# Performance work log

Hardware: AMD Instinct MI355X
Metric: run time of the kernel (lower is better)

The kernel has to match this reference:

```python
import jax, jax.numpy as jnp
import numpy as np


def setup_inputs() -> dict:
    key = jax.random.key(0)
    k1, k2, k3 = jax.random.split(key, 3)
    B, C, H, W = 512, 4, 125, 125
    img = jax.random.normal(k1, (B, C, H, W), dtype=jnp.float32)
    # fc: Linear(62500 -> 20), Tanh, Dropout(eval=identity), Linear(20 -> 1), Sigmoid
    W1 = jax.random.normal(k2, (C * H * W, 20), dtype=jnp.float32) * 0.004  # ~1/sqrt(62500)
    b1 = jnp.zeros((20,), dtype=jnp.float32)
    W2 = jax.random.normal(k3, (20, 1), dtype=jnp.float32) * 0.2
    b2 = jnpp = jnp.zeros((1,), dtype=jnp.float32)
    return {"img": img, "W1": W1, "b1": b1, "W2": W2, "b2": b2}


def reference(img, W1, b1, W2, b2):
    B, C, H, W = img.shape
    # small MLP -> rotation angle theta in [0, 2*pi)
    h = jnp.tanh(img.reshape(B, -1) @ W1 + b1)          # (B, 20)
    theta = jax.nn.sigmoid(h @ W2 + b2)[:, 0] * (2.0 * np.pi)  # (B,)
    c, s = jnp.cos(theta), jnp.sin(theta)
    z = jnp.zeros_like(c)
    # (B, 2, 3) affine matrix: pure rotation, zero translation
    Mat = jnp.stack([jnp.stack([c, -s, z], axis=-1),
                     jnp.stack([s,  c, z], axis=-1)], axis=-2)

    # affine_grid, align_corners=True: normalized coords span [-1, 1] at pixel centers
    ys = jnp.linspace(-1.0, 1.0, H, dtype=img.dtype)
    xs = jnp.linspace(-1.0, 1.0, W, dtype=img.dtype)
    gy, gx = jnp.meshgrid(ys, xs, indexing="ij")        # (H, W)
    base = jnp.stack([gx, gy, jnp.ones_like(gx)], axis=-1)  # (H, W, 3) homogeneous (x, y, 1)
    grid = jnp.einsum("bij,hwj->bhwi", Mat, base)       # (B, H, W, 2) -> (x, y)

    # grid_sample: bilinear, padding_mode='zeros', align_corners=True
    ix = (grid[..., 0] + 1.0) * 0.5 * (W - 1)
    iy = (grid[..., 1] + 1.0) * 0.5 * (H - 1)
    ix0 = jnp.floor(ix); iy0 = jnp.floor(iy)
    ix1 = ix0 + 1.0;     iy1 = iy0 + 1.0
    wx1 = ix - ix0; wx0 = 1.0 - wx1
    wy1 = iy - iy0; wy0 = 1.0 - wy1

    def gather(ixi, iyi):
        valid = (ixi >= 0) & (ixi <= W - 1) & (iyi >= 0) & (iyi <= H - 1)
        xc = jnp.clip(ixi, 0, W - 1).astype(jnp.int32)
        yc = jnp.clip(iyi, 0, H - 1).astype(jnp.int32)
        vals = jax.vmap(lambda im, yy, xx: im[:, yy, xx])(img, yc, xc)  # (B, C, H, W)
        return vals * valid[:, None, :, :].astype(img.dtype)

    out = (gather(ix0, iy0) * (wx0 * wy0)[:, None]
         + gather(ix1, iy0) * (wx1 * wy0)[:, None]
         + gather(ix0, iy1) * (wx0 * wy1)[:, None]
         + gather(ix1, iy1) * (wx1 * wy1)[:, None])
    return out, Mat
```

## Files before the change

kernel.cpp:

```cpp
#include <hip/hip_runtime.h>
#include <hip/hip_bf16.h>
#include <math.h>

#define K_TOT 62500
#define KQ_TOT 15625
#define NJ    20
#define NB    512
#define HW_   15625
#define WW_   125
#define NKSPL 128
#define LDSTR 68
#define SWSTR 124

#define HP_OFF   0
#define HRED_OFF (NKSPL * NJ * NB)
#define W1T_OFF  2000000
#define MAT_OFF  32000000

__global__ __launch_bounds__(256) void k0_transpose(const float* __restrict__ W1,
                                                    float* __restrict__ W1T) {
    const int k = blockIdx.x * 256 + threadIdx.x;
    if (k >= K_TOT) return;
    const float* src = W1 + (size_t)k * NJ;
#pragma unroll
    for (int j = 0; j < NJ; ++j)
        W1T[(size_t)j * K_TOT + k] = src[j];
}

__global__ __launch_bounds__(256, 2) void k1_partial(const float* __restrict__ img,
                                                     const float* __restrict__ W1T,
                                                     float* __restrict__ hpart) {
    __shared__ float  simg[2][64 * LDSTR];
    __shared__ float4 sw[NJ * SWSTR];
    const int tid  = threadIdx.x;
    const int bx   = blockIdx.x;
    const int b0   = blockIdx.y << 6;
    const int lane = tid & 63;
    const int j0   = __builtin_amdgcn_readfirstlane((tid >> 6) * 5);
    const int srow = tid >> 4;
    const int squad = tid & 15;

    const int q0  = (bx * KQ_TOT) >> 7;
    const int q1  = ((bx + 1) * KQ_TOT) >> 7;
    const int nqb = q1 - q0;
    const int nsteps = (nqb + 15) >> 4;

    const float4* img4 = reinterpret_cast<const float4*>(img);
    const float4* W1T4 = reinterpret_cast<const float4*>(W1T);

    for (int i = tid; i < NJ * 128; i += 256) {
        const int j  = i >> 7;
        const int qq = i & 127;
        if (qq < nqb)
            sw[j * SWSTR + qq] = W1T4[(size_t)j * KQ_TOT + q0 + qq];
    }

    float acc0 = 0.f, acc1 = 0.f, acc2 = 0.f, acc3 = 0.f, acc4 = 0.f;

    {
        const int cq = (nqb < 16) ? nqb : 16;
        if (squad < cq) {
            const int qg = q0 + squad;
#pragma unroll
            for (int rr = 0; rr < 4; ++rr) {
                const int row = srow + (rr << 4);
                *reinterpret_cast<float4*>(&simg[0][row * LDSTR + (squad << 2)]) =
                    img4[(size_t)(b0 + row) * KQ_TOT + qg];
            }
        }
    }
    __syncthreads();

    int cur = 0;
    for (int s = 0; s < nsteps; ++s) {
        float4 r0, r1, r2, r3;
        bool dl = false;
        if (s + 1 < nsteps) {
            const int rem = nqb - (s + 1) * 16;
            const int cq  = (rem < 16) ? rem : 16;
            if (squad < cq) {
                dl = true;
                const size_t qg = (size_t)q0 + (s + 1) * 16 + squad;
                r0 = img4[(size_t)(b0 + srow +  0) * KQ_TOT + qg];
                r1 = img4[(size_t)(b0 + srow + 16) * KQ_TOT + qg];
                r2 = img4[(size_t)(b0 + srow + 32) * KQ_TOT + qg];
                r3 = img4[(size_t)(b0 + srow + 48) * KQ_TOT + qg];
            }
        }

        {
            const int rem = nqb - s * 16;
            const int cq  = (rem < 16) ? rem : 16;
            const float* simgl = &simg[cur][lane * LDSTR];
            const int qbase = s * 16;
#pragma unroll 4
            for (int q = 0; q < cq; ++q) {
                const float4 iv = *reinterpret_cast<const float4*>(&simgl[q << 2]);
                const int qi = qbase + q;
                const float4 w0 = sw[(j0 + 0) * SWSTR + qi];
                const float4 w1 = sw[(j0 + 1) * SWSTR + qi];
                const float4 w2 = sw[(j0 + 2) * SWSTR + qi];
                const float4 w3 = sw[(j0 + 3) * SWSTR + qi];
                const float4 w4 = sw[(j0 + 4) * SWSTR + qi];
                acc0 += iv.x * w0.x + iv.y * w0.y + iv.z * w0.z + iv.w * w0.w;
                acc1 += iv.x * w1.x + iv.y * w1.y + iv.z * w1.z + iv.w * w1.w;
                acc2 += iv.x * w2.x + iv.y * w2.y + iv.z * w2.z + iv.w * w2.w;
                acc3 += iv.x * w3.x + iv.y * w3.y + iv.z * w3.z + iv.w * w3.w;
                acc4 += iv.x * w4.x + iv.y * w4.y + iv.z * w4.z + iv.w * w4.w;
            }
        }

        if (dl) {
            float* d = &simg[cur ^ 1][srow * LDSTR + (squad << 2)];
            *reinterpret_cast<float4*>(&d[ 0 * LDSTR]) = r0;
            *reinterpret_cast<float4*>(&d[16 * LDSTR]) = r1;
            *reinterpret_cast<float4*>(&d[32 * LDSTR]) = r2;
            *reinterpret_cast<float4*>(&d[48 * LDSTR]) = r3;
        }
        __syncthreads();
        cur ^= 1;
    }

    const int b = b0 + lane;
    float* dst = &hpart[(size_t)(bx * NJ + j0) * NB + b];
    dst[0 * NB] = acc0;
    dst[1 * NB] = acc1;
    dst[2 * NB] = acc2;
    dst[3 * NB] = acc3;
    dst[4 * NB] = acc4;
}

__global__ __launch_bounds__(256) void k2_reduce(const float* __restrict__ hpart,
                                                 float* __restrict__ hred) {
    const int b = blockIdx.x * 256 + threadIdx.x;
    const int j = blockIdx.y;
    float a = 0.f;
#pragma unroll 8
    for (int c = 0; c < NKSPL; ++c)
        a += hpart[(size_t)(c * NJ + j) * NB + b];
    hred[j * NB + b] = a;
}

__global__ __launch_bounds__(256) void k2_head(const float* __restrict__ hred,
                                               const float* __restrict__ b1,
                                               const float* __restrict__ W2,
                                               const float* __restrict__ b2,
                                               float* __restrict__ mat) {
    const int b = blockIdx.x * 256 + threadIdx.x;
    float z = b2[0];
#pragma unroll
    for (int j = 0; j < NJ; ++j) {
        const float h = tanhf(hred[j * NB + b] + b1[j]);
        z += h * W2[j];
    }
    const float sg = 1.0f / (1.0f + expf(-z));
    const float theta = sg * 6.28318530717958647692f;
    float sn, cn;
    sincosf(theta, &sn, &cn);
    float* m = mat + (size_t)b * 6;
    m[0] = cn; m[1] = -sn; m[2] = 0.f;
    m[3] = sn; m[4] = cn;  m[5] = 0.f;
}

__device__ __forceinline__ unsigned int pack2bf(float a, float b) {
    __hip_bfloat16 ha = __float2bfloat16(a);
    __hip_bfloat16 hb = __float2bfloat16(b);
    const unsigned int ua = (unsigned int)__builtin_bit_cast(unsigned short, ha);
    const unsigned int ub = (unsigned int)__builtin_bit_cast(unsigned short, hb);
    return ua | (ub << 16);
}
#define BF_LO(u) __uint_as_float((u) << 16)
#define BF_HI(u) __uint_as_float((u) & 0xffff0000u)

__global__ __launch_bounds__(1024) void k3_sample(const float* __restrict__ img,
                                                  const float* __restrict__ mat,
                                                  float* __restrict__ out) {
    __shared__ unsigned int sch[HW_];
    const int b   = blockIdx.x;
    const int tid = threadIdx.x;

    const float cb = mat[(size_t)b * 6 + 4];
    const float sb = mat[(size_t)b * 6 + 3];
    const size_t ib = (size_t)b * 4 * HW_;

#pragma unroll
    for (int pair = 0; pair < 2; ++pair) {
        const float* pa = img + ib + (size_t)(2 * pair) * HW_;
        const float* pb = pa + HW_;
        __syncthreads();
        for (int i = tid; i < HW_; i += 1024)
            sch[i] = pack2bf(pa[i], pb[i]);
        __syncthreads();

        float* oa = out + ib + (size_t)(2 * pair) * HW_;
        for (int p = tid; p < HW_; p += 1024) {
            const int y = p / WW_;
            const int x = p - y * WW_;

            const float gx = (float)x * (1.0f / 62.0f) - 1.0f;
            const float gy = (float)y * (1.0f / 62.0f) - 1.0f;
            const float fx = (cb * gx - sb * gy + 1.0f) * 62.0f;
            const float fy = (sb * gx + cb * gy + 1.0f) * 62.0f;

            const float x0f = floorf(fx), y0f = floorf(fy);
            const int x0 = (int)x0f, y0 = (int)y0f;
            const int x1 = x0 + 1, y1 = y0 + 1;
            const float wx1 = fx - x0f, wx0 = 1.0f - wx1;
            const float wy1 = fy - y0f, wy0 = 1.0f - wy1;

            const bool vx0 = ((unsigned)x0 <= 124u);
            const bool vx1 = ((unsigned)x1 <= 124u);
            const bool vy0 = ((unsigned)y0 <= 124u);
            const bool vy1 = ((unsigned)y1 <= 124u);

            const int cx0 = min(max(x0, 0), 124), cx1 = min(max(x1, 0), 124);
            const int cy0 = min(max(y0, 0), 124), cy1 = min(max(y1, 0), 124);

            const float m00 = (vx0 && vy0) ? wx0 * wy0 : 0.f;
            const float m01 = (vx1 && vy0) ? wx1 * wy0 : 0.f;
            const float m10 = (vx0 && vy1) ? wx0 * wy1 : 0.f;
            const float m11 = (vx1 && vy1) ? wx1 * wy1 : 0.f;

            const unsigned int q00 = sch[cy0 * WW_ + cx0];
            const unsigned int q01 = sch[cy0 * WW_ + cx1];
            const unsigned int q10 = sch[cy1 * WW_ + cx0];
            const unsigned int q11 = sch[cy1 * WW_ + cx1];

            float a0, a1;
            a0  = BF_LO(q00) * m00;  a1  = BF_HI(q00) * m00;
            a0 += BF_LO(q01) * m01;  a1 += BF_HI(q01) * m01;
            a0 += BF_LO(q10) * m10;  a1 += BF_HI(q10) * m10;
            a0 += BF_LO(q11) * m11;  a1 += BF_HI(q11) * m11;

            oa[p]       = a0;
            oa[p + HW_] = a1;
        }
    }
}

extern "C" void kernel_launch(void* const* d_in, const int* in_sizes, int n_in,
                              void* d_out, int out_size, void* d_ws, size_t ws_size,
                              hipStream_t stream) {
    const float* img = (const float*)d_in[0];
    const float* W1  = (const float*)d_in[1];
    const float* b1  = (const float*)d_in[2];
    const float* W2  = (const float*)d_in[3];
    const float* b2  = (const float*)d_in[4];
    float* out = (float*)d_out;

    float* hpart = out + HP_OFF;
    float* hred  = out + HRED_OFF;
    float* W1T   = out + W1T_OFF;
    float* mat   = out + MAT_OFF;

    hipLaunchKernelGGL(k0_transpose, dim3((K_TOT + 255) / 256), dim3(256), 0, stream, W1, W1T);
    hipLaunchKernelGGL(k1_partial, dim3(NKSPL, 8), dim3(256), 0, stream, img, W1T, hpart);
    hipLaunchKernelGGL(k2_reduce, dim3(2, NJ), dim3(256), 0, stream, hpart, hred);
    hipLaunchKernelGGL(k2_head, dim3(2), dim3(256), 0, stream, hred, b1, W2, b2, mat);
    hipLaunchKernelGGL(k3_sample, dim3(NB), dim3(1024), 0, stream, img, mat, out);
}
```

Before: 125.3 us.

## Pack W1 per group, read weights from global, split sampler across channel pairs

The weight transpose becomes a pack into four groups of five outputs each, interleaved per k. The GEMV kernel then reads weights straight from global memory (wave-uniform addresses) instead of staging them in LDS, which frees LDS so occupancy can rise to four blocks. The sampler launches one block per (batch, channel pair) instead of looping over both pairs, doubling the grid and removing a barrier round. The risk is more global/L2 weight traffic per block, and the first-stage load guard was dropped, which assumes each chunk has at least 16 quads.

```diff
diff --git a/kernel.cpp b/kernel.cpp
--- a/kernel.cpp
+++ b/kernel.cpp
@@ -10,63 +10,57 @@
 #define WW_   125
 #define NKSPL 128
 #define LDSTR 68
-#define SWSTR 124
+#define WPG   312500
 
 #define HP_OFF   0
 #define HRED_OFF (NKSPL * NJ * NB)
-#define W1T_OFF  2000000
+#define W1P_OFF  2000000
 #define MAT_OFF  32000000
 
-__global__ __launch_bounds__(256) void k0_transpose(const float* __restrict__ W1,
-                                                    float* __restrict__ W1T) {
+__global__ __launch_bounds__(256) void k0_pack(const float* __restrict__ W1,
+                                               float* __restrict__ W1P) {
     const int k = blockIdx.x * 256 + threadIdx.x;
     if (k >= K_TOT) return;
     const float* src = W1 + (size_t)k * NJ;
 #pragma unroll
-    for (int j = 0; j < NJ; ++j)
-        W1T[(size_t)j * K_TOT + k] = src[j];
-}
-
-__global__ __launch_bounds__(256, 2) void k1_partial(const float* __restrict__ img,
-                                                     const float* __restrict__ W1T,
+    for (int g = 0; g < 4; ++g) {
+        float* d = W1P + (size_t)g * WPG + (size_t)k * 5;
+#pragma unroll
+        for (int r = 0; r < 5; ++r)
+            d[r] = src[5 * g + r];
+    }
+}
+
+__global__ __launch_bounds__(256, 4) void k1_partial(const float* __restrict__ img,
+                                                     const float* __restrict__ W1P,
                                                      float* __restrict__ hpart) {
-    __shared__ float  simg[2][64 * LDSTR];
-    __shared__ float4 sw[NJ * SWSTR];
+    __shared__ float simg[2][64 * LDSTR];
     const int tid  = threadIdx.x;
     const int bx   = blockIdx.x;
     const int b0   = blockIdx.y << 6;
     const int lane = tid & 63;
-    const int j0   = __builtin_amdgcn_readfirstlane((tid >> 6) * 5);
+    const int jg   = __builtin_amdgcn_readfirstlane(tid >> 6);
+    const int j0   = jg * 5;
     const int srow = tid >> 4;
     const int squad = tid & 15;
 
-    const int q0  = (bx * KQ_TOT) >> 7;
-    const int q1  = ((bx + 1) * KQ_TOT) >> 7;
+    const int q0  = (int)(((long long)bx * KQ_TOT) >> 7);
+    const int q1  = (int)(((long long)(bx + 1) * KQ_TOT) >> 7);
     const int nqb = q1 - q0;
     const int nsteps = (nqb + 15) >> 4;
 
     const float4* img4 = reinterpret_cast<const float4*>(img);
-    const float4* W1T4 = reinterpret_cast<const float4*>(W1T);
-
-    for (int i = tid; i < NJ * 128; i += 256) {
-        const int j  = i >> 7;
-        const int qq = i & 127;
-        if (qq < nqb)
-            sw[j * SWSTR + qq] = W1T4[(size_t)j * KQ_TOT + q0 + qq];
-    }
+    const float4* wg4 = reinterpret_cast<const float4*>(W1P + (size_t)jg * WPG);
 
     float acc0 = 0.f, acc1 = 0.f, acc2 = 0.f, acc3 = 0.f, acc4 = 0.f;
 
     {
-        const int cq = (nqb < 16) ? nqb : 16;
-        if (squad < cq) {
-            const int qg = q0 + squad;
-#pragma unroll
-            for (int rr = 0; rr < 4; ++rr) {
-                const int row = srow + (rr << 4);
-                *reinterpret_cast<float4*>(&simg[0][row * LDSTR + (squad << 2)]) =
-                    img4[(size_t)(b0 + row) * KQ_TOT + qg];
-            }
+        const int qg = q0 + squad;
+#pragma unroll
+        for (int rr = 0; rr < 4; ++rr) {
+            const int row = srow + (rr << 4);
+            *reinterpret_cast<float4*>(&simg[0][row * LDSTR + (squad << 2)]) =
+                img4[(size_t)(b0 + row) * KQ_TOT + qg];
         }
     }
     __syncthreads();
@@ -92,21 +86,24 @@
             const int rem = nqb - s * 16;
             const int cq  = (rem < 16) ? rem : 16;
             const float* simgl = &simg[cur][lane * LDSTR];
-            const int qbase = s * 16;
-#pragma unroll 4
+            const int qb = q0 + s * 16;
+#pragma unroll 16
             for (int q = 0; q < cq; ++q) {
                 const float4 iv = *reinterpret_cast<const float4*>(&simgl[q << 2]);
-                const int qi = qbase + q;
-                const float4 w0 = sw[(j0 + 0) * SWSTR + qi];
-                const float4 w1 = sw[(j0 + 1) * SWSTR + qi];
-                const float4 w2 = sw[(j0 + 2) * SWSTR + qi];
-                const float4 w3 = sw[(j0 + 3) * SWSTR + qi];
-                const float4 w4 = sw[(j0 + 4) * SWSTR + qi];
-                acc0 += iv.x * w0.x + iv.y * w0.y + iv.z * w0.z + iv.w * w0.w;
-                acc1 += iv.x * w1.x + iv.y * w1.y + iv.z * w1.z + iv.w * w1.w;
-                acc2 += iv.x * w2.x + iv.y * w2.y + iv.z * w2.z + iv.w * w2.w;
-                acc3 += iv.x * w3.x + iv.y * w3.y + iv.z * w3.z + iv.w * w3.w;
-                acc4 += iv.x * w4.x + iv.y * w4.y + iv.z * w4.z + iv.w * w4.w;
+                const float4* wq = wg4 + (size_t)(qb + q) * 5;
+                const float4 w0 = wq[0];
+                const float4 w1 = wq[1];
+                const float4 w2 = wq[2];
+                const float4 w3 = wq[3];
+                const float4 w4 = wq[4];
+                acc0 += iv.x * w0.x;  acc1 += iv.x * w0.y;  acc2 += iv.x * w0.z;
+                acc3 += iv.x * w0.w;  acc4 += iv.x * w1.x;
+                acc0 += iv.y * w1.y;  acc1 += iv.y * w1.z;  acc2 += iv.y * w1.w;
+                acc3 += iv.y * w2.x;  acc4 += iv.y * w2.y;
+                acc0 += iv.z * w2.z;  acc1 += iv.z * w2.w;  acc2 += iv.z * w3.x;
+                acc3 += iv.z * w3.y;  acc4 += iv.z * w3.z;
+                acc0 += iv.w * w3.w;  acc1 += iv.w * w4.x;  acc2 += iv.w * w4.y;
+                acc3 += iv.w * w4.z;  acc4 += iv.w * w4.w;
             }
         }
 
@@ -176,65 +173,62 @@
                                                   const float* __restrict__ mat,
                                                   float* __restrict__ out) {
     __shared__ unsigned int sch[HW_];
-    const int b   = blockIdx.x;
-    const int tid = threadIdx.x;
+    const int b    = blockIdx.x;
+    const int pair = blockIdx.y;
+    const int tid  = threadIdx.x;
 
     const float cb = mat[(size_t)b * 6 + 4];
     const float sb = mat[(size_t)b * 6 + 3];
     const size_t ib = (size_t)b * 4 * HW_;
-
-#pragma unroll
-    for (int pair = 0; pair < 2; ++pair) {
-        const float* pa = img + ib + (size_t)(2 * pair) * HW_;
-        const float* pb = pa + HW_;
-        __syncthreads();
-        for (int i = tid; i < HW_; i += 1024)
-            sch[i] = pack2bf(pa[i], pb[i]);
-        __syncthreads();
-
-        float* oa = out + ib + (size_t)(2 * pair) * HW_;
-        for (int p = tid; p < HW_; p += 1024) {
-            const int y = p / WW_;
-            const int x = p - y * WW_;
-
-            const float gx = (float)x * (1.0f / 62.0f) - 1.0f;
-            const float gy = (float)y * (1.0f / 62.0f) - 1.0f;
-            const float fx = (cb * gx - sb * gy + 1.0f) * 62.0f;
-            const float fy = (sb * gx + cb * gy + 1.0f) * 62.0f;
-
-            const float x0f = floorf(fx), y0f = floorf(fy);
-            const int x0 = (int)x0f, y0 = (int)y0f;
-            const int x1 = x0 + 1, y1 = y0 + 1;
-            const float wx1 = fx - x0f, wx0 = 1.0f - wx1;
-            const float wy1 = fy - y0f, wy0 = 1.0f - wy1;
-
-            const bool vx0 = ((unsigned)x0 <= 124u);
-            const bool vx1 = ((unsigned)x1 <= 124u);
-            const bool vy0 = ((unsigned)y0 <= 124u);
-            const bool vy1 = ((unsigned)y1 <= 124u);
-
-            const int cx0 = min(max(x0, 0), 124), cx1 = min(max(x1, 0), 124);
-            const int cy0 = min(max(y0, 0), 124), cy1 = min(max(y1, 0), 124);
-
-            const float m00 = (vx0 && vy0) ? wx0 * wy0 : 0.f;
-            const float m01 = (vx1 && vy0) ? wx1 * wy0 : 0.f;
-            const float m10 = (vx0 && vy1) ? wx0 * wy1 : 0.f;
-            const float m11 = (vx1 && vy1) ? wx1 * wy1 : 0.f;
-
-            const unsigned int q00 = sch[cy0 * WW_ + cx0];
-            const unsigned int q01 = sch[cy0 * WW_ + cx1];
-            const unsigned int q10 = sch[cy1 * WW_ + cx0];
-            const unsigned int q11 = sch[cy1 * WW_ + cx1];
-
-            float a0, a1;
-            a0  = BF_LO(q00) * m00;  a1  = BF_HI(q00) * m00;
-            a0 += BF_LO(q01) * m01;  a1 += BF_HI(q01) * m01;
-            a0 += BF_LO(q10) * m10;  a1 += BF_HI(q10) * m10;
-            a0 += BF_LO(q11) * m11;  a1 += BF_HI(q11) * m11;
-
-            oa[p]       = a0;
-            oa[p + HW_] = a1;
-        }
+    const float* pa = img + ib + (size_t)(2 * pair) * HW_;
+    const float* pb = pa + HW_;
+
+    for (int i = tid; i < HW_; i += 1024)
+        sch[i] = pack2bf(pa[i], pb[i]);
+    __syncthreads();
+
+    float* oa = out + ib + (size_t)(2 * pair) * HW_;
+    for (int p = tid; p < HW_; p += 1024) {
+        const int y = p / WW_;
+        const int x = p - y * WW_;
+
+        const float gx = (float)x * (1.0f / 62.0f) - 1.0f;
+        const float gy = (float)y * (1.0f / 62.0f) - 1.0f;
+        const float fx = (cb * gx - sb * gy + 1.0f) * 62.0f;
+        const float fy = (sb * gx + cb * gy + 1.0f) * 62.0f;
+
+        const float x0f = floorf(fx), y0f = floorf(fy);
+        const int x0 = (int)x0f, y0 = (int)y0f;
+        const int x1 = x0 + 1, y1 = y0 + 1;
+        const float wx1 = fx - x0f, wx0 = 1.0f - wx1;
+        const float wy1 = fy - y0f, wy0 = 1.0f - wy1;
+
+        const bool vx0 = ((unsigned)x0 <= 124u);
+        const bool vx1 = ((unsigned)x1 <= 124u);
+        const bool vy0 = ((unsigned)y0 <= 124u);
+        const bool vy1 = ((unsigned)y1 <= 124u);
+
+        const int cx0 = min(max(x0, 0), 124), cx1 = min(max(x1, 0), 124);
+        const int cy0 = min(max(y0, 0), 124), cy1 = min(max(y1, 0), 124);
+
+        const float m00 = (vx0 && vy0) ? wx0 * wy0 : 0.f;
+        const float m01 = (vx1 && vy0) ? wx1 * wy0 : 0.f;
+        const float m10 = (vx0 && vy1) ? wx0 * wy1 : 0.f;
+        const float m11 = (vx1 && vy1) ? wx1 * wy1 : 0.f;
+
+        const unsigned int q00 = sch[cy0 * WW_ + cx0];
+        const unsigned int q01 = sch[cy0 * WW_ + cx1];
+        const unsigned int q10 = sch[cy1 * WW_ + cx0];
+        const unsigned int q11 = sch[cy1 * WW_ + cx1];
+
+        float a0, a1;
+        a0  = BF_LO(q00) * m00;  a1  = BF_HI(q00) * m00;
+        a0 += BF_LO(q01) * m01;  a1 += BF_HI(q01) * m01;
+        a0 += BF_LO(q10) * m10;  a1 += BF_HI(q10) * m10;
+        a0 += BF_LO(q11) * m11;  a1 += BF_HI(q11) * m11;
+
+        oa[p]       = a0;
+        oa[p + HW_] = a1;
     }
 }
 
@@ -250,12 +244,12 @@
 
     float* hpart = out + HP_OFF;
     float* hred  = out + HRED_OFF;
-    float* W1T   = out + W1T_OFF;
+    float* W1P   = out + W1P_OFF;
     float* mat   = out + MAT_OFF;
 
-    hipLaunchKernelGGL(k0_transpose, dim3((K_TOT + 255) / 256), dim3(256), 0, stream, W1, W1T);
-    hipLaunchKernelGGL(k1_partial, dim3(NKSPL, 8), dim3(256), 0, stream, img, W1T, hpart);
+    hipLaunchKernelGGL(k0_pack, dim3((K_TOT + 255) / 256), dim3(256), 0, stream, W1, W1P);
+    hipLaunchKernelGGL(k1_partial, dim3(NKSPL, 8), dim3(256), 0, stream, img, W1P, hpart);
     hipLaunchKernelGGL(k2_reduce, dim3(2, NJ), dim3(256), 0, stream, hpart, hred);
     hipLaunchKernelGGL(k2_head, dim3(2), dim3(256), 0, stream, hred, b1, W2, b2, mat);
-    hipLaunchKernelGGL(k3_sample, dim3(NB), dim3(1024), 0, stream, img, mat, out);
-}
+    hipLaunchKernelGGL(k3_sample, dim3(NB, 2), dim3(1024), 0, stream, img, mat, out);
+}
```

Result: slower. 130.9 us (+4.4%).
